# Kernel tuning notes

Measured on AMD Instinct MI355X. Metric: run time of the kernel, lower is better.

## Reference

```python
import jax, jax.numpy as jnp
import numpy as np

B, L, S, E, H = 2, 2048, 2048, 1024, 16
D = E // H


def setup_inputs() -> dict:
    key = jax.random.key(0)
    ks = jax.random.split(key, 16)
    p = 0.02  # small init scale for weights
    return {
        "a": jax.random.normal(ks[0], (B, L, E), jnp.float32),
        "b": jax.random.normal(ks[1], (B, S, E), jnp.float32),
        "Wa_qk": jax.random.normal(ks[2], (E, E), jnp.float32) * p,
        "ba_qk": jax.random.normal(ks[3], (E,), jnp.float32) * p,
        "Wa_v": jax.random.normal(ks[4], (E, E), jnp.float32) * p,
        "ba_v": jax.random.normal(ks[5], (E,), jnp.float32) * p,
        "Wb_qk": jax.random.normal(ks[6], (E, E), jnp.float32) * p,
        "bb_qk": jax.random.normal(ks[7], (E,), jnp.float32) * p,
        "Wb_v": jax.random.normal(ks[8], (E, E), jnp.float32) * p,
        "bb_v": jax.random.normal(ks[9], (E,), jnp.float32) * p,
        "Wa_o": jax.random.normal(ks[10], (E, E), jnp.float32) * p,
        "ba_o": jax.random.normal(ks[11], (E,), jnp.float32) * p,
        "Wb_o": jax.random.normal(ks[12], (E, E), jnp.float32) * p,
        "bb_o": jax.random.normal(ks[13], (E,), jnp.float32) * p,
    }


def _heads(x, n, W, bias):
    # x: [B, N, E] -> projected and split to [B, H, N, D]
    y = x @ W + bias
    return y.reshape(B, n, H, D).transpose(0, 2, 1, 3)


def reference(a, b, Wa_qk, ba_qk, Wa_v, ba_v, Wb_qk, bb_qk, Wb_v, bb_v,
              Wa_o, ba_o, Wb_o, bb_o):
    aq = _heads(a, L, Wa_qk, ba_qk)   # [B,H,L,D]
    av = _heads(a, L, Wa_v, ba_v)     # [B,H,L,D]
    bq = _heads(b, S, Wb_qk, bb_qk)   # [B,H,S,D]
    bv = _heads(b, S, Wb_v, bb_v)     # [B,H,S,D]

    scale = 1.0 / jnp.sqrt(jnp.float32(D))
    # Shared score matrix [B,H,L,S]
    scores = jnp.einsum('bhld,bhsd->bhls', aq, bq) * scale
    # Dual softmax: row-wise (over S) and column-wise (over L)
    wa = jax.nn.softmax(scores, axis=-1)                    # [B,H,L,S]
    wb = jax.nn.softmax(scores, axis=-2).transpose(0, 1, 3, 2)  # [B,H,S,L]

    a_ctx = jnp.einsum('bhls,bhsd->bhld', wa, bv)  # [B,H,L,D]
    b_ctx = jnp.einsum('bhsl,bhld->bhsd', wb, av)  # [B,H,S,D]

    a_out = a_ctx.transpose(0, 2, 1, 3).reshape(B, L, E) @ Wa_o + ba_o
    b_out = b_ctx.transpose(0, 2, 1, 3).reshape(B, S, E) @ Wb_o + bb_o
    return (a_out, b_out)
```

## Files before the change

### kernel.cpp

```cpp
#include <hip/hip_runtime.h>
#include <hip/hip_bf16.h>
#include <stdint.h>

typedef unsigned short u16;
typedef unsigned int u32;
typedef __attribute__((ext_vector_type(8))) short bf16x8;
typedef __attribute__((ext_vector_type(4))) float f32x4;

typedef __attribute__((address_space(3))) void lds_void;
typedef const __attribute__((address_space(1))) void gbl_void;

#define SIDE 4194304u
#define BHSTR 131072u

static __device__ __forceinline__ u16 f2bf(float f) {
  union { __hip_bfloat16 b; u16 u; } cv;
  cv.b = __float2bfloat16(f);
  return cv.u;
}
static __device__ __forceinline__ float bf2f(u16 u) {
  union { __hip_bfloat16 b; u16 u; } cv;
  cv.u = u;
  return __bfloat162float(cv.b);
}

__global__ __launch_bounds__(256) void k_cvt_in(const float* __restrict__ a,
                                                const float* __restrict__ b,
                                                u16* __restrict__ dst) {
  int z = blockIdx.y;
  const float* src = z ? b : a;
  size_t i = ((size_t)blockIdx.x * 256 + threadIdx.x) * 8;
  float4 x0 = *(const float4*)(src + i);
  float4 x1 = *(const float4*)(src + i + 4);
  u16 t[8] = {f2bf(x0.x), f2bf(x0.y), f2bf(x0.z), f2bf(x0.w),
              f2bf(x1.x), f2bf(x1.y), f2bf(x1.z), f2bf(x1.w)};
  *(uint4*)(dst + (size_t)z * SIDE + i) = *(uint4*)t;
}

__global__ __launch_bounds__(256) void k_cvt_bias(
    const float* s0, const float* s1, const float* s2, const float* s3,
    const float* s4, const float* s5, u16* __restrict__ dst) {
  const float* srcs[6] = {s0, s1, s2, s3, s4, s5};
  int z = blockIdx.y;
  int i = blockIdx.x * 256 + threadIdx.x;
  float sc = (z == 0) ? 0.125f : 1.0f;
  dst[z * 1024 + i] = f2bf(srcs[z][i] * sc);
}

__global__ __launch_bounds__(256) void k_transpose_w(
    const float* a0, const float* a1, const float* a2, const float* a3,
    const float* a4, const float* a5,
    u16* d0, u16* d1, u16* d2, u16* d3, u16* d4, u16* d5) {
  __shared__ u16 tile[64][72];
  const float* srcs[6] = {a0, a1, a2, a3, a4, a5};
  u16* dsts[6] = {d0, d1, d2, d3, d4, d5};
  int z = blockIdx.z;
  float sc = (z == 0) ? 0.125f : 1.0f;
  const float* src = srcs[z] + (size_t)(blockIdx.y * 64) * 1024 + blockIdx.x * 64;
  int t = threadIdx.x;
  int row = t >> 2, c4 = t & 3;
#pragma unroll
  for (int p = 0; p < 2; ++p) {
    int col = c4 * 8 + p * 32;
    const float* sf = src + (size_t)row * 1024 + col;
    float4 x0 = *(const float4*)sf;
    float4 x1 = *(const float4*)(sf + 4);
    u16 tmp[8] = {f2bf(x0.x * sc), f2bf(x0.y * sc), f2bf(x0.z * sc), f2bf(x0.w * sc),
                  f2bf(x1.x * sc), f2bf(x1.y * sc), f2bf(x1.z * sc), f2bf(x1.w * sc)};
    *(uint4*)(&tile[row][col]) = *(uint4*)tmp;
  }
  __syncthreads();
  u16* dst = dsts[z] + (size_t)(blockIdx.x * 64) * 1024 + blockIdx.y * 64;
#pragma unroll
  for (int p = 0; p < 2; ++p) {
    int col = c4 * 8 + p * 32;
    u16 tmp[8];
#pragma unroll
    for (int i = 0; i < 8; ++i) tmp[i] = tile[col + i][row];
    *(uint4*)(dst + (size_t)row * 1024 + col) = *(uint4*)tmp;
  }
}

__global__ __launch_bounds__(256) void k_gemm_qkv(
    const u16* __restrict__ Aall, const u16* __restrict__ WtA,
    const u16* __restrict__ WtB, const u16* __restrict__ bias,
    u16* __restrict__ qkbuf, u16* __restrict__ vbuf) {
  __shared__ u16 Sh[8192];
  u16* As = Sh;
  u16* Bs = Sh + 4096;
  int tid = threadIdx.x;
  int wave = tid >> 6, lane = tid & 63;
  int quad = lane >> 4, lrow = lane & 15;
  int wr = wave >> 1, wc = wave & 1;
  int z = blockIdx.z;
  int m0 = blockIdx.y * 128, n0 = blockIdx.x * 128;
  const u16* A = Aall + (size_t)z * SIDE;
  const u16* Wt = z ? WtB : WtA;
  const u16* bi = bias + (size_t)z * 2048;

  f32x4 acc[4][4] = {};
  int srow = 32 * wave + (lane >> 2);
  int scol = (lane & 3) * 8;
  const u16* gA = A + (size_t)(m0 + srow) * 1024 + scol;
  const u16* gB = Wt + (size_t)(n0 + srow) * 1024 + scol;
  u16* lA = &As[(32 * wave) * 32];
  u16* lB = &Bs[(32 * wave) * 32];

  for (int k0 = 0; k0 < 1024; k0 += 32) {
    __syncthreads();
#pragma unroll
    for (int j = 0; j < 2; ++j) {
      __builtin_amdgcn_global_load_lds((gbl_void*)(gA + (size_t)(16 * j) * 1024 + k0),
                                       (lds_void*)(lA + 16 * j * 32), 16, 0, 0);
      __builtin_amdgcn_global_load_lds((gbl_void*)(gB + (size_t)(16 * j) * 1024 + k0),
                                       (lds_void*)(lB + 16 * j * 32), 16, 0, 0);
    }
    __syncthreads();
    bf16x8 af[4], bfr[4];
#pragma unroll
    for (int i = 0; i < 4; ++i)
      af[i] = *(const bf16x8*)&As[(64 * wr + 16 * i + lrow) * 32 + 8 * quad];
#pragma unroll
    for (int j = 0; j < 4; ++j)
      bfr[j] = *(const bf16x8*)&Bs[(64 * wc + 16 * j + lrow) * 32 + 8 * quad];
#pragma unroll
    for (int i = 0; i < 4; ++i)
#pragma unroll
      for (int j = 0; j < 4; ++j)
        acc[i][j] = __builtin_amdgcn_mfma_f32_16x16x32_bf16(af[i], bfr[j], acc[i][j], 0, 0, 0);
  }

  float bv[4];
#pragma unroll
  for (int j = 0; j < 4; ++j) bv[j] = bf2f(bi[n0 + 64 * wc + 16 * j + lrow]);

  int x = blockIdx.x;
  bool isv = (x >= 8);
  int h = (isv ? 2 * (x - 8) : 2 * x) + wc;
  u16* dst = (isv ? vbuf : qkbuf) + (size_t)z * SIDE;
  u16* lw = Sh + wave * 1216;

  __syncthreads();
#pragma unroll
  for (int i = 0; i < 4; ++i) {
#pragma unroll
    for (int j = 0; j < 4; ++j)
#pragma unroll
      for (int r = 0; r < 4; ++r)
        lw[(4 * quad + r) * 76 + 16 * j + lrow] = f2bf(acc[i][j][r] + bv[j]);
    asm volatile("s_waitcnt lgkmcnt(0)" ::: "memory");
    int row = lane >> 2, cg = (lane & 3) * 16;
    int rg = m0 + 64 * wr + 16 * i + row;
    int bb = rg >> 11, rl = rg & 2047;
    u16* dr = dst + (size_t)(bb * 16 + h) * BHSTR + (size_t)rl * 64 + cg;
    uint2 w0 = *(const uint2*)&lw[row * 76 + cg];
    uint2 w1 = *(const uint2*)&lw[row * 76 + cg + 4];
    uint2 w2 = *(const uint2*)&lw[row * 76 + cg + 8];
    uint2 w3 = *(const uint2*)&lw[row * 76 + cg + 12];
    uint4 o0 = {w0.x, w0.y, w1.x, w1.y};
    uint4 o1 = {w2.x, w2.y, w3.x, w3.y};
    *(uint4*)dr = o0;
    *(uint4*)(dr + 8) = o1;
    asm volatile("s_waitcnt lgkmcnt(0)" ::: "memory");
  }
}

__global__ __launch_bounds__(256) void k_transpose_v(const u16* __restrict__ v,
                                                     u16* __restrict__ vt) {
  __shared__ u16 tile[64][72];
  int sbh = blockIdx.y;
  int n0 = blockIdx.x * 64;
  const u16* src = v + (size_t)sbh * BHSTR + (size_t)n0 * 64;
  u16* dst = vt + (size_t)sbh * BHSTR + n0;
  int t = threadIdx.x;
  int row = t >> 2, c4 = t & 3;
#pragma unroll
  for (int p = 0; p < 2; ++p) {
    int col = c4 * 8 + p * 32;
    uint4 q = *(const uint4*)(src + (size_t)row * 64 + col);
    *(uint4*)(&tile[row][col]) = q;
  }
  __syncthreads();
#pragma unroll
  for (int p = 0; p < 2; ++p) {
    int col = c4 * 8 + p * 32;
    u16 tmp[8];
#pragma unroll
    for (int i = 0; i < 8; ++i) tmp[i] = tile[col + i][row];
    *(uint4*)(dst + (size_t)row * 2048 + col) = *(uint4*)tmp;
  }
}

__global__ __launch_bounds__(256) void k_attn(
    const u16* __restrict__ qk, const u16* __restrict__ vt,
    u16* __restrict__ ctx) {
  __shared__ u16 Ks[2 * 4096];
  __shared__ u16 Vs[2 * 4096];
  __shared__ u16 Ps[128 * 64];
  int tid = threadIdx.x;
  int wave = tid >> 6, lane = tid & 63;
  int quad = lane >> 4, lrow = lane & 15;
  int z = blockIdx.z, bh = blockIdx.x;
  int l0 = blockIdx.y * 128;
  const u16* Qb = qk + (size_t)z * SIDE + (size_t)bh * BHSTR + (size_t)l0 * 64;
  const u16* Kb = qk + (size_t)(1 - z) * SIDE + (size_t)bh * BHSTR;
  const u16* Vtb = vt + (size_t)(1 - z) * SIDE + (size_t)bh * BHSTR;

#pragma unroll
  for (int p = 0; p < 4; ++p) {
    int G0 = wave * 256 + p * 64;
    int G = G0 + lane;
    int row = G >> 3, c = G & 7;
    __builtin_amdgcn_global_load_lds((gbl_void*)(Qb + (size_t)row * 64 + ((c ^ (row & 7)) * 8)),
                                     (lds_void*)(Ps + G0 * 8), 16, 0, 0);
  }
#pragma unroll
  for (int p = 0; p < 2; ++p) {
    int G0 = p * 256 + wave * 64;
    int G = G0 + lane;
    int row = G >> 3, c = G & 7;
    int sw = (c ^ (row & 7)) * 8;
    __builtin_amdgcn_global_load_lds((gbl_void*)(Kb + (size_t)row * 64 + sw),
                                     (lds_void*)(Ks + G0 * 8), 16, 0, 0);
    __builtin_amdgcn_global_load_lds((gbl_void*)(Vtb + (size_t)row * 2048 + sw),
                                     (lds_void*)(Vs + G0 * 8), 16, 0, 0);
  }

  bf16x8 qf[2][2];
  f32x4 cacc[2][4] = {};
  float rsum[2] = {0.f, 0.f};
  int e = 2 * (lrow & 7);

  for (int it = 0; it < 32; ++it) {
    __syncthreads();
    if (it == 0) {
#pragma unroll
      for (int rt = 0; rt < 2; ++rt) {
        int lq = 32 * wave + 16 * rt + lrow;
        qf[rt][0] = *(const bf16x8*)&Ps[(lq * 8 + (quad ^ (lq & 7))) * 8];
        qf[rt][1] = *(const bf16x8*)&Ps[(lq * 8 + ((quad + 4) ^ (lq & 7))) * 8];
      }
    }
    int prty = it & 1;
    if (it + 1 < 32) {
      int s1 = (it + 1) << 6;
      int nb = (1 - prty) * 4096;
#pragma unroll
      for (int p = 0; p < 2; ++p) {
        int G0 = p * 256 + wave * 64;
        int G = G0 + lane;
        int row = G >> 3, c = G & 7;
        int sw = (c ^ (row & 7)) * 8;
        __builtin_amdgcn_global_load_lds((gbl_void*)(Kb + (size_t)(s1 + row) * 64 + sw),
                                         (lds_void*)(Ks + nb + G0 * 8), 16, 0, 0);
        __builtin_amdgcn_global_load_lds((gbl_void*)(Vtb + (size_t)row * 2048 + s1 + sw),
                                         (lds_void*)(Vs + nb + G0 * 8), 16, 0, 0);
      }
    }
    const u16* KsC = Ks + prty * 4096;
    const u16* VsC = Vs + prty * 4096;
#pragma unroll
    for (int j = 0; j < 4; ++j) {
      int kr = 16 * j + lrow;
      bf16x8 kf0 = *(const bf16x8*)&KsC[(kr * 8 + (quad ^ (kr & 7))) * 8];
      bf16x8 kf1 = *(const bf16x8*)&KsC[(kr * 8 + ((quad + 4) ^ (kr & 7))) * 8];
#pragma unroll
      for (int rt = 0; rt < 2; ++rt) {
        f32x4 s = {};
        s = __builtin_amdgcn_mfma_f32_16x16x32_bf16(kf0, qf[rt][0], s, 0, 0, 0);
        s = __builtin_amdgcn_mfma_f32_16x16x32_bf16(kf1, qf[rt][1], s, 0, 0, 0);
        float e0 = __expf(s[0]), e1 = __expf(s[1]);
        float e2 = __expf(s[2]), e3 = __expf(s[3]);
        rsum[rt] += (e0 + e1) + (e2 + e3);
        uint2 pk;
        pk.x = ((u32)f2bf(e1) << 16) | (u32)f2bf(e0);
        pk.y = ((u32)f2bf(e3) << 16) | (u32)f2bf(e2);
        *(uint2*)&Ps[(32 * wave + 16 * rt + lrow) * 64 + ((4 * j + quad) ^ e) * 4] = pk;
      }
    }
    asm volatile("s_waitcnt lgkmcnt(0)" ::: "memory");
    bf16x8 pf[2][2];
#pragma unroll
    for (int rt = 0; rt < 2; ++rt) {
      const u16* pr = &Ps[(32 * wave + 16 * rt + lrow) * 64];
      pf[rt][0] = *(const bf16x8*)&pr[((2 * quad) ^ e) * 4];
      pf[rt][1] = *(const bf16x8*)&pr[((2 * quad + 8) ^ e) * 4];
    }
#pragma unroll
    for (int j = 0; j < 4; ++j) {
      int vr = 16 * j + lrow;
      bf16x8 vf0 = *(const bf16x8*)&VsC[(vr * 8 + (quad ^ (vr & 7))) * 8];
      bf16x8 vf1 = *(const bf16x8*)&VsC[(vr * 8 + ((quad + 4) ^ (vr & 7))) * 8];
#pragma unroll
      for (int rt = 0; rt < 2; ++rt) {
        cacc[rt][j] = __builtin_amdgcn_mfma_f32_16x16x32_bf16(pf[rt][0], vf0, cacc[rt][j], 0, 0, 0);
        cacc[rt][j] = __builtin_amdgcn_mfma_f32_16x16x32_bf16(pf[rt][1], vf1, cacc[rt][j], 0, 0, 0);
      }
    }
  }

  float rinv[2][4];
#pragma unroll
  for (int rt = 0; rt < 2; ++rt) {
    float v = rsum[rt];
    v += __shfl_xor(v, 16);
    v += __shfl_xor(v, 32);
    float rv = 1.0f / v;
#pragma unroll
    for (int r = 0; r < 4; ++r)
      rinv[rt][r] = __shfl(rv, 20 * quad + r);
  }

  int bb = bh >> 4, h = bh & 15;
  u16* Ob = ctx + (size_t)z * SIDE + (size_t)(bb * 2048 + l0) * 1024 + h * 64;
#pragma unroll
  for (int rt = 0; rt < 2; ++rt)
#pragma unroll
    for (int r = 0; r < 4; ++r) {
      int l = 32 * wave + 16 * rt + 4 * quad + r;
#pragma unroll
      for (int j = 0; j < 4; ++j)
        Ob[(size_t)l * 1024 + 16 * j + lrow] = f2bf(cacc[rt][j][r] * rinv[rt][r]);
    }
}

__global__ __launch_bounds__(256) void k_gemm_o(
    const u16* __restrict__ ctx, const u16* __restrict__ WtO,
    const u16* __restrict__ bias, float* __restrict__ out) {
  __shared__ u16 As[128 * 32];
  __shared__ u16 Bs[128 * 32];
  int tid = threadIdx.x;
  int wave = tid >> 6, lane = tid & 63;
  int quad = lane >> 4, lrow = lane & 15;
  int wr = wave >> 1, wc = wave & 1;
  int z = blockIdx.z;
  int m0 = blockIdx.y * 128, n0 = blockIdx.x * 128;
  const u16* A = ctx + (size_t)z * SIDE;
  const u16* Wt = WtO + (size_t)z * 1048576;
  const u16* bi = bias + (size_t)z * 1024;
  float* C = out + (size_t)z * SIDE;

  f32x4 acc[4][4] = {};
  int srow = 32 * wave + (lane >> 2);
  int scol = (lane & 3) * 8;
  const u16* gA = A + (size_t)(m0 + srow) * 1024 + scol;
  const u16* gB = Wt + (size_t)(n0 + srow) * 1024 + scol;
  u16* lA = &As[(32 * wave) * 32];
  u16* lB = &Bs[(32 * wave) * 32];

  for (int k0 = 0; k0 < 1024; k0 += 32) {
    __syncthreads();
#pragma unroll
    for (int j = 0; j < 2; ++j) {
      __builtin_amdgcn_global_load_lds((gbl_void*)(gA + (size_t)(16 * j) * 1024 + k0),
                                       (lds_void*)(lA + 16 * j * 32), 16, 0, 0);
      __builtin_amdgcn_global_load_lds((gbl_void*)(gB + (size_t)(16 * j) * 1024 + k0),
                                       (lds_void*)(lB + 16 * j * 32), 16, 0, 0);
    }
    __syncthreads();
    bf16x8 af[4], bfr[4];
#pragma unroll
    for (int i = 0; i < 4; ++i)
      af[i] = *(const bf16x8*)&As[(64 * wr + 16 * i + lrow) * 32 + 8 * quad];
#pragma unroll
    for (int j = 0; j < 4; ++j)
      bfr[j] = *(const bf16x8*)&Bs[(64 * wc + 16 * j + lrow) * 32 + 8 * quad];
#pragma unroll
    for (int i = 0; i < 4; ++i)
#pragma unroll
      for (int j = 0; j < 4; ++j)
        acc[i][j] = __builtin_amdgcn_mfma_f32_16x16x32_bf16(af[i], bfr[j], acc[i][j], 0, 0, 0);
  }

  float bv[4];
#pragma unroll
  for (int j = 0; j < 4; ++j) bv[j] = bf2f(bi[n0 + 64 * wc + 16 * j + lrow]);
#pragma unroll
  for (int i = 0; i < 4; ++i) {
    int row = m0 + 64 * wr + 16 * i + 4 * quad;
#pragma unroll
    for (int j = 0; j < 4; ++j) {
      int col = n0 + 64 * wc + 16 * j + lrow;
#pragma unroll
      for (int r = 0; r < 4; ++r)
        C[(size_t)(row + r) * 1024 + col] = acc[i][j][r] + bv[j];
    }
  }
}

extern "C" void kernel_launch(void* const* d_in, const int* in_sizes, int n_in,
                              void* d_out, int out_size, void* d_ws, size_t ws_size,
                              hipStream_t stream) {
  (void)in_sizes; (void)n_in; (void)out_size; (void)ws_size;
  const size_t M1 = 1048576u;
  u16* ws = (u16*)d_ws;
  u16* wtA   = ws;
  u16* wtB   = ws + 2 * M1;
  u16* wtO   = ws + 4 * M1;
  u16* biasQ = ws + 6 * M1;
  u16* biasO = ws + 6 * M1 + 4096;
  u16* ab    = ws + 7 * M1;
  u16* vt    = ab;
  u16* qkbuf = ws + 15 * M1;
  u16* vbuf  = ws + 23 * M1;
  u16* ctx   = vbuf;

  dim3 blk(256);
  k_cvt_in<<<dim3(2048, 2), blk, 0, stream>>>((const float*)d_in[0],
                                              (const float*)d_in[1], ab);
  k_cvt_bias<<<dim3(4, 6), blk, 0, stream>>>(
      (const float*)d_in[3], (const float*)d_in[5], (const float*)d_in[7],
      (const float*)d_in[9], (const float*)d_in[11], (const float*)d_in[13], biasQ);
  k_transpose_w<<<dim3(16, 16, 6), blk, 0, stream>>>(
      (const float*)d_in[2], (const float*)d_in[4], (const float*)d_in[6],
      (const float*)d_in[8], (const float*)d_in[10], (const float*)d_in[12],
      wtA, wtA + M1, wtB, wtB + M1, wtO, wtO + M1);
  k_gemm_qkv<<<dim3(16, 32, 2), blk, 0, stream>>>(ab, wtA, wtB, biasQ, qkbuf, vbuf);
  k_transpose_v<<<dim3(32, 64), blk, 0, stream>>>(vbuf, vt);
  k_attn<<<dim3(32, 16, 2), blk, 0, stream>>>(qkbuf, vt, ctx);
  k_gemm_o<<<dim3(8, 32, 2), blk, 0, stream>>>(ctx, wtO, biasO, (float*)d_out);
}
```

Measured before the change: 316.6 us.

## Double query tile per attention block, use exp2 and MFMA row sums

The attention kernel now handles 256 query rows per block (64 per wave) instead of 128. This halves the number of K/V tile loads per query and doubles the MFMA work per staged tile. Q fragments are loaded straight from global memory into registers, and the log2(e) factor is folded into the Q weight scale so exp2f can replace __expf. Row sums are now accumulated with an MFMA against a ones vector, which removes the per-element adds and the cross-lane shuffles. The costs are higher register pressure from the larger accumulators (a launch bound of 2 is requested), fewer blocks in the grid, and row sums computed from the bf16-rounded probabilities.

```diff
diff --git a/kernel.cpp b/kernel.cpp
--- a/kernel.cpp
+++ b/kernel.cpp
@@ -43,7 +43,7 @@
   const float* srcs[6] = {s0, s1, s2, s3, s4, s5};
   int z = blockIdx.y;
   int i = blockIdx.x * 256 + threadIdx.x;
-  float sc = (z == 0) ? 0.125f : 1.0f;
+  float sc = (z == 0) ? 0.18033688011112042f : 1.0f;
   dst[z * 1024 + i] = f2bf(srcs[z][i] * sc);
 }
 
@@ -55,7 +55,7 @@
   const float* srcs[6] = {a0, a1, a2, a3, a4, a5};
   u16* dsts[6] = {d0, d1, d2, d3, d4, d5};
   int z = blockIdx.z;
-  float sc = (z == 0) ? 0.125f : 1.0f;
+  float sc = (z == 0) ? 0.18033688011112042f : 1.0f;
   const float* src = srcs[z] + (size_t)(blockIdx.y * 64) * 1024 + blockIdx.x * 64;
   int t = threadIdx.x;
   int row = t >> 2, c4 = t & 3;
@@ -191,29 +191,29 @@
   }
 }
 
-__global__ __launch_bounds__(256) void k_attn(
+__global__ __launch_bounds__(256, 2) void k_attn(
     const u16* __restrict__ qk, const u16* __restrict__ vt,
     u16* __restrict__ ctx) {
   __shared__ u16 Ks[2 * 4096];
   __shared__ u16 Vs[2 * 4096];
-  __shared__ u16 Ps[128 * 64];
+  __shared__ u16 Ps[4 * 4096];
   int tid = threadIdx.x;
   int wave = tid >> 6, lane = tid & 63;
   int quad = lane >> 4, lrow = lane & 15;
   int z = blockIdx.z, bh = blockIdx.x;
-  int l0 = blockIdx.y * 128;
+  int l0 = blockIdx.y * 256;
   const u16* Qb = qk + (size_t)z * SIDE + (size_t)bh * BHSTR + (size_t)l0 * 64;
   const u16* Kb = qk + (size_t)(1 - z) * SIDE + (size_t)bh * BHSTR;
   const u16* Vtb = vt + (size_t)(1 - z) * SIDE + (size_t)bh * BHSTR;
 
-#pragma unroll
-  for (int p = 0; p < 4; ++p) {
-    int G0 = wave * 256 + p * 64;
-    int G = G0 + lane;
-    int row = G >> 3, c = G & 7;
-    __builtin_amdgcn_global_load_lds((gbl_void*)(Qb + (size_t)row * 64 + ((c ^ (row & 7)) * 8)),
-                                     (lds_void*)(Ps + G0 * 8), 16, 0, 0);
-  }
+  bf16x8 qf[4][2];
+#pragma unroll
+  for (int rt = 0; rt < 4; ++rt) {
+    int lq = 64 * wave + 16 * rt + lrow;
+    qf[rt][0] = *(const bf16x8*)&Qb[(size_t)lq * 64 + 8 * quad];
+    qf[rt][1] = *(const bf16x8*)&Qb[(size_t)lq * 64 + 32 + 8 * quad];
+  }
+
 #pragma unroll
   for (int p = 0; p < 2; ++p) {
     int G0 = p * 256 + wave * 64;
@@ -226,21 +226,20 @@
                                      (lds_void*)(Vs + G0 * 8), 16, 0, 0);
   }
 
-  bf16x8 qf[2][2];
-  f32x4 cacc[2][4] = {};
-  float rsum[2] = {0.f, 0.f};
+  bf16x8 ones;
+  {
+    short o = 0x3F80;
+#pragma unroll
+    for (int i = 0; i < 8; ++i) ones[i] = o;
+  }
+
+  f32x4 cacc[4][4] = {};
+  f32x4 asum[4] = {};
   int e = 2 * (lrow & 7);
+  u16* Pw = Ps + wave * 4096;
 
   for (int it = 0; it < 32; ++it) {
     __syncthreads();
-    if (it == 0) {
-#pragma unroll
-      for (int rt = 0; rt < 2; ++rt) {
-        int lq = 32 * wave + 16 * rt + lrow;
-        qf[rt][0] = *(const bf16x8*)&Ps[(lq * 8 + (quad ^ (lq & 7))) * 8];
-        qf[rt][1] = *(const bf16x8*)&Ps[(lq * 8 + ((quad + 4) ^ (lq & 7))) * 8];
-      }
-    }
     int prty = it & 1;
     if (it + 1 < 32) {
       int s1 = (it + 1) << 6;
@@ -265,24 +264,23 @@
       bf16x8 kf0 = *(const bf16x8*)&KsC[(kr * 8 + (quad ^ (kr & 7))) * 8];
       bf16x8 kf1 = *(const bf16x8*)&KsC[(kr * 8 + ((quad + 4) ^ (kr & 7))) * 8];
 #pragma unroll
-      for (int rt = 0; rt < 2; ++rt) {
+      for (int rt = 0; rt < 4; ++rt) {
         f32x4 s = {};
         s = __builtin_amdgcn_mfma_f32_16x16x32_bf16(kf0, qf[rt][0], s, 0, 0, 0);
         s = __builtin_amdgcn_mfma_f32_16x16x32_bf16(kf1, qf[rt][1], s, 0, 0, 0);
-        float e0 = __expf(s[0]), e1 = __expf(s[1]);
-        float e2 = __expf(s[2]), e3 = __expf(s[3]);
-        rsum[rt] += (e0 + e1) + (e2 + e3);
+        float e0 = exp2f(s[0]), e1 = exp2f(s[1]);
+        float e2 = exp2f(s[2]), e3 = exp2f(s[3]);
         uint2 pk;
         pk.x = ((u32)f2bf(e1) << 16) | (u32)f2bf(e0);
         pk.y = ((u32)f2bf(e3) << 16) | (u32)f2bf(e2);
-        *(uint2*)&Ps[(32 * wave + 16 * rt + lrow) * 64 + ((4 * j + quad) ^ e) * 4] = pk;
+        *(uint2*)&Pw[(16 * rt + lrow) * 64 + ((4 * j + quad) ^ e) * 4] = pk;
       }
     }
     asm volatile("s_waitcnt lgkmcnt(0)" ::: "memory");
-    bf16x8 pf[2][2];
-#pragma unroll
-    for (int rt = 0; rt < 2; ++rt) {
-      const u16* pr = &Ps[(32 * wave + 16 * rt + lrow) * 64];
+    bf16x8 pf[4][2];
+#pragma unroll
+    for (int rt = 0; rt < 4; ++rt) {
+      const u16* pr = &Pw[(16 * rt + lrow) * 64];
       pf[rt][0] = *(const bf16x8*)&pr[((2 * quad) ^ e) * 4];
       pf[rt][1] = *(const bf16x8*)&pr[((2 * quad + 8) ^ e) * 4];
     }
@@ -292,36 +290,31 @@
       bf16x8 vf0 = *(const bf16x8*)&VsC[(vr * 8 + (quad ^ (vr & 7))) * 8];
       bf16x8 vf1 = *(const bf16x8*)&VsC[(vr * 8 + ((quad + 4) ^ (vr & 7))) * 8];
 #pragma unroll
-      for (int rt = 0; rt < 2; ++rt) {
+      for (int rt = 0; rt < 4; ++rt) {
         cacc[rt][j] = __builtin_amdgcn_mfma_f32_16x16x32_bf16(pf[rt][0], vf0, cacc[rt][j], 0, 0, 0);
         cacc[rt][j] = __builtin_amdgcn_mfma_f32_16x16x32_bf16(pf[rt][1], vf1, cacc[rt][j], 0, 0, 0);
       }
     }
-  }
-
-  float rinv[2][4];
-#pragma unroll
-  for (int rt = 0; rt < 2; ++rt) {
-    float v = rsum[rt];
-    v += __shfl_xor(v, 16);
-    v += __shfl_xor(v, 32);
-    float rv = 1.0f / v;
-#pragma unroll
-    for (int r = 0; r < 4; ++r)
-      rinv[rt][r] = __shfl(rv, 20 * quad + r);
+#pragma unroll
+    for (int rt = 0; rt < 4; ++rt) {
+      asum[rt] = __builtin_amdgcn_mfma_f32_16x16x32_bf16(pf[rt][0], ones, asum[rt], 0, 0, 0);
+      asum[rt] = __builtin_amdgcn_mfma_f32_16x16x32_bf16(pf[rt][1], ones, asum[rt], 0, 0, 0);
+    }
   }
 
   int bb = bh >> 4, h = bh & 15;
   u16* Ob = ctx + (size_t)z * SIDE + (size_t)(bb * 2048 + l0) * 1024 + h * 64;
 #pragma unroll
-  for (int rt = 0; rt < 2; ++rt)
+  for (int rt = 0; rt < 4; ++rt) {
 #pragma unroll
     for (int r = 0; r < 4; ++r) {
-      int l = 32 * wave + 16 * rt + 4 * quad + r;
+      float rinv = 1.0f / asum[rt][r];
+      int l = 64 * wave + 16 * rt + 4 * quad + r;
 #pragma unroll
       for (int j = 0; j < 4; ++j)
-        Ob[(size_t)l * 1024 + 16 * j + lrow] = f2bf(cacc[rt][j][r] * rinv[rt][r]);
-    }
+        Ob[(size_t)l * 1024 + 16 * j + lrow] = f2bf(cacc[rt][j][r] * rinv);
+    }
+  }
 }
 
 __global__ __launch_bounds__(256) void k_gemm_o(
@@ -417,6 +410,6 @@
       wtA, wtA + M1, wtB, wtB + M1, wtO, wtO + M1);
   k_gemm_qkv<<<dim3(16, 32, 2), blk, 0, stream>>>(ab, wtA, wtB, biasQ, qkbuf, vbuf);
   k_transpose_v<<<dim3(32, 64), blk, 0, stream>>>(vbuf, vt);
-  k_attn<<<dim3(32, 16, 2), blk, 0, stream>>>(qkbuf, vt, ctx);
+  k_attn<<<dim3(32, 8, 2), blk, 0, stream>>>(qkbuf, vt, ctx);
   k_gemm_o<<<dim3(8, 32, 2), blk, 0, stream>>>(ctx, wtO, biasO, (float*)d_out);
 }
```

Result: slower. 330.2 us (+4.3%).

## Double GEMM K-tile with XOR-swizzled LDS and fold log2e into exp2

Applied to the files above, without the earlier changes.

Both projection GEMMs now stage 64-wide K tiles per barrier pair instead of 32, halving the number of __syncthreads rounds. The LDS layout gets an XOR swizzle so the wider rows read without bank conflicts. Separately, log2(e) is folded into the query weight/bias scale so the attention softmax can use exp2f instead of __expf. The cost is doubled LDS per block, which may lower occupancy, and slightly different bf16 rounding of the pre-scaled weights.

```diff
diff --git a/kernel.cpp b/kernel.cpp
--- a/kernel.cpp
+++ b/kernel.cpp
@@ -43,7 +43,7 @@
   const float* srcs[6] = {s0, s1, s2, s3, s4, s5};
   int z = blockIdx.y;
   int i = blockIdx.x * 256 + threadIdx.x;
-  float sc = (z == 0) ? 0.125f : 1.0f;
+  float sc = (z == 0) ? 0.18033688011112042f : 1.0f;
   dst[z * 1024 + i] = f2bf(srcs[z][i] * sc);
 }
 
@@ -55,7 +55,7 @@
   const float* srcs[6] = {a0, a1, a2, a3, a4, a5};
   u16* dsts[6] = {d0, d1, d2, d3, d4, d5};
   int z = blockIdx.z;
-  float sc = (z == 0) ? 0.125f : 1.0f;
+  float sc = (z == 0) ? 0.18033688011112042f : 1.0f;
   const float* src = srcs[z] + (size_t)(blockIdx.y * 64) * 1024 + blockIdx.x * 64;
   int t = threadIdx.x;
   int row = t >> 2, c4 = t & 3;
@@ -85,9 +85,9 @@
     const u16* __restrict__ Aall, const u16* __restrict__ WtA,
     const u16* __restrict__ WtB, const u16* __restrict__ bias,
     u16* __restrict__ qkbuf, u16* __restrict__ vbuf) {
-  __shared__ u16 Sh[8192];
+  __shared__ u16 Sh[16384];
   u16* As = Sh;
-  u16* Bs = Sh + 4096;
+  u16* Bs = Sh + 8192;
   int tid = threadIdx.x;
   int wave = tid >> 6, lane = tid & 63;
   int quad = lane >> 4, lrow = lane & 15;
@@ -99,35 +99,40 @@
   const u16* bi = bias + (size_t)z * 2048;
 
   f32x4 acc[4][4] = {};
-  int srow = 32 * wave + (lane >> 2);
-  int scol = (lane & 3) * 8;
-  const u16* gA = A + (size_t)(m0 + srow) * 1024 + scol;
-  const u16* gB = Wt + (size_t)(n0 + srow) * 1024 + scol;
-  u16* lA = &As[(32 * wave) * 32];
-  u16* lB = &Bs[(32 * wave) * 32];
-
-  for (int k0 = 0; k0 < 1024; k0 += 32) {
+  int srow = 32 * wave + (lane >> 3);
+  int sgr = lane & 7;
+  int ssw = (sgr ^ (lane >> 3)) * 8;
+  const u16* gA = A + (size_t)(m0 + srow) * 1024 + ssw;
+  const u16* gB = Wt + (size_t)(n0 + srow) * 1024 + ssw;
+  u16* lA = &As[(32 * wave) * 64];
+  u16* lB = &Bs[(32 * wave) * 64];
+
+  for (int k0 = 0; k0 < 1024; k0 += 64) {
     __syncthreads();
 #pragma unroll
-    for (int j = 0; j < 2; ++j) {
-      __builtin_amdgcn_global_load_lds((gbl_void*)(gA + (size_t)(16 * j) * 1024 + k0),
-                                       (lds_void*)(lA + 16 * j * 32), 16, 0, 0);
-      __builtin_amdgcn_global_load_lds((gbl_void*)(gB + (size_t)(16 * j) * 1024 + k0),
-                                       (lds_void*)(lB + 16 * j * 32), 16, 0, 0);
+    for (int j = 0; j < 4; ++j) {
+      __builtin_amdgcn_global_load_lds((gbl_void*)(gA + (size_t)(8 * j) * 1024 + k0),
+                                       (lds_void*)(lA + 8 * j * 64), 16, 0, 0);
+      __builtin_amdgcn_global_load_lds((gbl_void*)(gB + (size_t)(8 * j) * 1024 + k0),
+                                       (lds_void*)(lB + 8 * j * 64), 16, 0, 0);
     }
     __syncthreads();
-    bf16x8 af[4], bfr[4];
-#pragma unroll
-    for (int i = 0; i < 4; ++i)
-      af[i] = *(const bf16x8*)&As[(64 * wr + 16 * i + lrow) * 32 + 8 * quad];
-#pragma unroll
-    for (int j = 0; j < 4; ++j)
-      bfr[j] = *(const bf16x8*)&Bs[(64 * wc + 16 * j + lrow) * 32 + 8 * quad];
-#pragma unroll
-    for (int i = 0; i < 4; ++i)
+#pragma unroll
+    for (int kk = 0; kk < 2; ++kk) {
+      int gq = ((kk << 2) + quad) ^ (lrow & 7);
+      bf16x8 af[4], bfr[4];
+#pragma unroll
+      for (int i = 0; i < 4; ++i)
+        af[i] = *(const bf16x8*)&As[(64 * wr + 16 * i + lrow) * 64 + gq * 8];
 #pragma unroll
       for (int j = 0; j < 4; ++j)
-        acc[i][j] = __builtin_amdgcn_mfma_f32_16x16x32_bf16(af[i], bfr[j], acc[i][j], 0, 0, 0);
+        bfr[j] = *(const bf16x8*)&Bs[(64 * wc + 16 * j + lrow) * 64 + gq * 8];
+#pragma unroll
+      for (int i = 0; i < 4; ++i)
+#pragma unroll
+        for (int j = 0; j < 4; ++j)
+          acc[i][j] = __builtin_amdgcn_mfma_f32_16x16x32_bf16(af[i], bfr[j], acc[i][j], 0, 0, 0);
+    }
   }
 
   float bv[4];
@@ -269,8 +274,8 @@
         f32x4 s = {};
         s = __builtin_amdgcn_mfma_f32_16x16x32_bf16(kf0, qf[rt][0], s, 0, 0, 0);
         s = __builtin_amdgcn_mfma_f32_16x16x32_bf16(kf1, qf[rt][1], s, 0, 0, 0);
-        float e0 = __expf(s[0]), e1 = __expf(s[1]);
-        float e2 = __expf(s[2]), e3 = __expf(s[3]);
+        float e0 = exp2f(s[0]), e1 = exp2f(s[1]);
+        float e2 = exp2f(s[2]), e3 = exp2f(s[3]);
         rsum[rt] += (e0 + e1) + (e2 + e3);
         uint2 pk;
         pk.x = ((u32)f2bf(e1) << 16) | (u32)f2bf(e0);
@@ -327,8 +332,8 @@
 __global__ __launch_bounds__(256) void k_gemm_o(
     const u16* __restrict__ ctx, const u16* __restrict__ WtO,
     const u16* __restrict__ bias, float* __restrict__ out) {
-  __shared__ u16 As[128 * 32];
-  __shared__ u16 Bs[128 * 32];
+  __shared__ u16 As[128 * 64];
+  __shared__ u16 Bs[128 * 64];
   int tid = threadIdx.x;
   int wave = tid >> 6, lane = tid & 63;
   int quad = lane >> 4, lrow = lane & 15;
@@ -341,35 +346,39 @@
   float* C = out + (size_t)z * SIDE;
 
   f32x4 acc[4][4] = {};
-  int srow = 32 * wave + (lane >> 2);
-  int scol = (lane & 3) * 8;
-  const u16* gA = A + (size_t)(m0 + srow) * 1024 + scol;
-  const u16* gB = Wt + (size_t)(n0 + srow) * 1024 + scol;
-  u16* lA = &As[(32 * wave) * 32];
-  u16* lB = &Bs[(32 * wave) * 32];
-
-  for (int k0 = 0; k0 < 1024; k0 += 32) {
+  int srow = 32 * wave + (lane >> 3);
+  int ssw = ((lane & 7) ^ (lane >> 3)) * 8;
+  const u16* gA = A + (size_t)(m0 + srow) * 1024 + ssw;
+  const u16* gB = Wt + (size_t)(n0 + srow) * 1024 + ssw;
+  u16* lA = &As[(32 * wave) * 64];
+  u16* lB = &Bs[(32 * wave) * 64];
+
+  for (int k0 = 0; k0 < 1024; k0 += 64) {
     __syncthreads();
 #pragma unroll
-    for (int j = 0; j < 2; ++j) {
-      __builtin_amdgcn_global_load_lds((gbl_void*)(gA + (size_t)(16 * j) * 1024 + k0),
-                                       (lds_void*)(lA + 16 * j * 32), 16, 0, 0);
-      __builtin_amdgcn_global_load_lds((gbl_void*)(gB + (size_t)(16 * j) * 1024 + k0),
-                                       (lds_void*)(lB + 16 * j * 32), 16, 0, 0);
+    for (int j = 0; j < 4; ++j) {
+      __builtin_amdgcn_global_load_lds((gbl_void*)(gA + (size_t)(8 * j) * 1024 + k0),
+                                       (lds_void*)(lA + 8 * j * 64), 16, 0, 0);
+      __builtin_amdgcn_global_load_lds((gbl_void*)(gB + (size_t)(8 * j) * 1024 + k0),
+                                       (lds_void*)(lB + 8 * j * 64), 16, 0, 0);
     }
     __syncthreads();
-    bf16x8 af[4], bfr[4];
-#pragma unroll
-    for (int i = 0; i < 4; ++i)
-      af[i] = *(const bf16x8*)&As[(64 * wr + 16 * i + lrow) * 32 + 8 * quad];
-#pragma unroll
-    for (int j = 0; j < 4; ++j)
-      bfr[j] = *(const bf16x8*)&Bs[(64 * wc + 16 * j + lrow) * 32 + 8 * quad];
-#pragma unroll
-    for (int i = 0; i < 4; ++i)
+#pragma unroll
+    for (int kk = 0; kk < 2; ++kk) {
+      int gq = ((kk << 2) + quad) ^ (lrow & 7);
+      bf16x8 af[4], bfr[4];
+#pragma unroll
+      for (int i = 0; i < 4; ++i)
+        af[i] = *(const bf16x8*)&As[(64 * wr + 16 * i + lrow) * 64 + gq * 8];
 #pragma unroll
       for (int j = 0; j < 4; ++j)
-        acc[i][j] = __builtin_amdgcn_mfma_f32_16x16x32_bf16(af[i], bfr[j], acc[i][j], 0, 0, 0);
+        bfr[j] = *(const bf16x8*)&Bs[(64 * wc + 16 * j + lrow) * 64 + gq * 8];
+#pragma unroll
+      for (int i = 0; i < 4; ++i)
+#pragma unroll
+        for (int j = 0; j < 4; ++j)
+          acc[i][j] = __builtin_amdgcn_mfma_f32_16x16x32_bf16(af[i], bfr[j], acc[i][j], 0, 0, 0);
+    }
   }
 
   float bv[4];
```

Result: no change. 321.0 us (+1.4%).
